# Optimization experiments

Hardware: AMD Instinct MI355X
Metric: run time of the kernel (lower is better)

The kernel has to match this reference:

```python
import jax, jax.numpy as jnp
import numpy as np

N_NODES = 200000
N_EVENTS = 200000
MEM_DIM = 128
MSG_DIM = 128
TIME_DIM = 16
MSG_IN = 2 * MEM_DIM + MSG_DIM + TIME_DIM  # 400


def setup_inputs() -> dict:
    key = jax.random.key(0)
    ks = jax.random.split(key, 12)
    return {
        "src_ids": jax.random.randint(ks[0], (N_EVENTS,), 0, N_NODES, dtype=jnp.int32),
        "dst_ids": jax.random.randint(ks[1], (N_EVENTS,), 0, N_NODES, dtype=jnp.int32),
        "edge_feat": jax.random.normal(ks[2], (N_EVENTS, MSG_DIM), dtype=jnp.float32),
        "timestamps": jax.random.uniform(ks[3], (N_EVENTS,), dtype=jnp.float32),
        "memory": jax.random.normal(ks[4], (N_NODES, MEM_DIM), dtype=jnp.float32) * 0.1,
        "last_update_time": jnp.zeros((N_NODES,), dtype=jnp.float32),
        "time_w": jax.random.normal(ks[5], (TIME_DIM,), dtype=jnp.float32),
        "time_phi": jnp.zeros((TIME_DIM,), dtype=jnp.float32),
        "W1": jax.random.normal(ks[6], (MSG_IN, MSG_DIM), dtype=jnp.float32) / np.sqrt(MSG_IN),
        "b1": jnp.zeros((MSG_DIM,), dtype=jnp.float32),
        "W2": jax.random.normal(ks[7], (MSG_DIM, MSG_DIM), dtype=jnp.float32) / np.sqrt(MSG_DIM),
        "b2": jnp.zeros((MSG_DIM,), dtype=jnp.float32),
        "W_ih": jax.random.normal(ks[8], (3 * MEM_DIM, MSG_DIM), dtype=jnp.float32) / np.sqrt(MSG_DIM),
        "W_hh": jax.random.normal(ks[9], (3 * MEM_DIM, MEM_DIM), dtype=jnp.float32) / np.sqrt(MEM_DIM),
        "b_ih": jnp.zeros((3 * MEM_DIM,), dtype=jnp.float32),
        "b_hh": jnp.zeros((3 * MEM_DIM,), dtype=jnp.float32),
    }


def _time_encode(dt, w, phi):
    # Time2Vec: linear first channel, sin on the rest
    wt = dt[:, None] * w[None, :] + phi[None, :]  # [E, TIME_DIM]
    return jnp.concatenate([wt[:, :1], jnp.sin(wt[:, 1:])], axis=-1)


def _message_mlp(x, W1, b1, W2, b2):
    h = jax.nn.relu(x @ W1 + b1)
    return h @ W2 + b2


def _gru_cell(x, h, W_ih, W_hh, b_ih, b_hh):
    gi = x @ W_ih.T + b_ih  # [U, 3H]
    gh = h @ W_hh.T + b_hh
    i_r, i_z, i_n = jnp.split(gi, 3, axis=-1)
    h_r, h_z, h_n = jnp.split(gh, 3, axis=-1)
    r = jax.nn.sigmoid(i_r + h_r)
    z = jax.nn.sigmoid(i_z + h_z)
    n = jnp.tanh(i_n + r * h_n)
    return (1.0 - z) * n + z * h


def reference(src_ids, dst_ids, edge_feat, timestamps, memory, last_update_time,
              time_w, time_phi, W1, b1, W2, b2, W_ih, W_hh, b_ih, b_hh):
    # 1) gather + time encode
    dt_src = timestamps - last_update_time[src_ids]
    dt_dst = timestamps - last_update_time[dst_ids]
    te_src = _time_encode(dt_src, time_w, time_phi)
    te_dst = _time_encode(dt_dst, time_w, time_phi)
    src_mem = memory[src_ids]
    dst_mem = memory[dst_ids]

    # 2) messages
    msg_src = _message_mlp(jnp.concatenate([src_mem, dst_mem, edge_feat, te_src], -1), W1, b1, W2, b2)
    msg_dst = _message_mlp(jnp.concatenate([dst_mem, src_mem, edge_feat, te_dst], -1), W1, b1, W2, b2)

    all_nodes = jnp.concatenate([src_ids, dst_ids])  # [2E]
    all_msgs = jnp.concatenate([msg_src, msg_dst], axis=0)  # [2E, MSG_DIM]

    # 3) 'last' aggregation: segment-max of positions, then gather
    pos = jnp.arange(all_nodes.shape[0], dtype=jnp.int32)
    last_pos = jax.ops.segment_max(pos, all_nodes, num_segments=N_NODES)  # int32 min where absent
    present = last_pos >= 0  # [N]
    agg = all_msgs[jnp.clip(last_pos, 0, None)]  # [N, MSG_DIM]
    agg = jnp.where(present[:, None], agg, 0.0)

    # 4) GRU memory update on involved nodes only
    new_mem = _gru_cell(agg, memory, W_ih, W_hh, b_ih, b_hh)
    memory_out = jnp.where(present[:, None], new_mem, memory)
    return memory_out
```

## Files before the change

### kernel.cpp

```cpp
#include <hip/hip_runtime.h>
#include <hip/hip_bf16.h>
#include <math.h>

#define NN 200000
#define NE 200000

typedef __attribute__((ext_vector_type(8))) short bf16x8;
typedef __attribute__((ext_vector_type(4))) float f32x4;

#define XASTR 136
#define XBSTR 296
#define OSTR  132
#define NT    (NN / 32)
#define PBT   (32 * XBSTR)

__device__ __forceinline__ float sigm(float x) { return 1.0f / (1.0f + __expf(-x)); }
__device__ __forceinline__ float tanh_f(float x) {
    float e = __expf(2.0f * x);
    return 1.0f - 2.0f / (e + 1.0f);
}
__device__ __forceinline__ ushort f2b(float x) {
    union { __hip_bfloat16 b; ushort u; } v;
    v.b = __float2bfloat16(x);
    return v.u;
}
__device__ __forceinline__ float b2f(ushort u) {
    return __uint_as_float(((unsigned)u) << 16);
}
__device__ __forceinline__ ushort4 cvt4(float4 v) {
    ushort4 u; u.x = f2b(v.x); u.y = f2b(v.y); u.z = f2b(v.z); u.w = f2b(v.w);
    return u;
}
__device__ __forceinline__ void gload_lds16(const ushort* g, ushort* l) {
    __builtin_amdgcn_global_load_lds(
        (const __attribute__((address_space(1))) unsigned int*)g,
        (__attribute__((address_space(3))) unsigned int*)l, 16, 0, 0);
}

#define MFMA16(a, b, c) __builtin_amdgcn_mfma_f32_16x16x32_bf16((a), (b), (c), 0, 0, 0)

__global__ void k_prep(const float* __restrict__ W1, const float* __restrict__ W2,
                       const float* __restrict__ Wih, const float* __restrict__ Whh,
                       const float* __restrict__ b2, const float* __restrict__ bih,
                       ushort* __restrict__ W1F, ushort* __restrict__ W2IF,
                       ushort* __restrict__ WHF, float* __restrict__ cb) {
    int t = blockIdx.x * 256 + threadIdx.x;
    if (t < 104 * 512) {
        int f = t >> 9, idx = t & 511;
        int lane = idx >> 3, j = idx & 7, c16 = lane & 15, k8 = lane >> 4;
        int wvv = f / 26, r = f % 26, kt = r >> 1, ns = r & 1;
        int col = wvv * 32 + ns * 16 + c16;
        int kk = kt * 32 + k8 * 8 + j;
        W1F[t] = (kk < 400) ? f2b(W1[kk * 128 + col]) : (ushort)0;
        return;
    }
    t -= 104 * 512;
    if (t < 96 * 512) {
        int f = t >> 9, idx = t & 511;
        int lane = idx >> 3, j = idx & 7, c16 = lane & 15, k8 = lane >> 4;
        int wvv = f / 24, r = f % 24, kt = r / 6, rem = r % 6, g = rem >> 1, ns = rem & 1;
        int col = g * 128 + wvv * 32 + ns * 16 + c16;
        int kk = kt * 32 + k8 * 8 + j;
        float s = 0.0f;
        for (int c = 0; c < 128; ++c) s = fmaf(W2[kk * 128 + c], Wih[col * 128 + c], s);
        W2IF[f * 512 + idx] = f2b(s);
        return;
    }
    t -= 96 * 512;
    if (t < 96 * 512) {
        int f = t >> 9, idx = t & 511;
        int lane = idx >> 3, j = idx & 7, c16 = lane & 15, k8 = lane >> 4;
        int wvv = f / 24, r = f % 24, kt = r / 6, rem = r % 6, g = rem >> 1, ns = rem & 1;
        int col = g * 128 + wvv * 32 + ns * 16 + c16;
        int kk = kt * 32 + k8 * 8 + j;
        WHF[f * 512 + idx] = f2b(Whh[col * 128 + kk]);
        return;
    }
    t -= 96 * 512;
    if (t < 384) {
        float s = bih[t];
        for (int k = 0; k < 128; ++k) s = fmaf(b2[k], Wih[t * 128 + k], s);
        cb[t] = s;
    }
}

__global__ void k_scatter(const int* __restrict__ src, const int* __restrict__ dst,
                          int* __restrict__ last_pos) {
    int i = blockIdx.x * blockDim.x + threadIdx.x;
    if (i < NE) {
        atomicMax(&last_pos[src[i]], i);
    } else if (i < 2 * NE) {
        atomicMax(&last_pos[dst[i - NE]], i);
    }
}

__global__ __launch_bounds__(256)
void k_gath(const int* __restrict__ last_pos,
            const int* __restrict__ src, const int* __restrict__ dst,
            const float* __restrict__ ts, const float* __restrict__ lut,
            const float* __restrict__ mem, const float* __restrict__ ef,
            const float* __restrict__ tw, const float* __restrict__ tphi,
            ushort* __restrict__ PB)
{
    const int wv = threadIdx.x >> 6, lane = threadIdx.x & 63;
    const int n0 = (blockIdx.x * 4 + wv) * 2;
    const int l = lane - 32;
    #pragma unroll
    for (int s = 0; s < 2; ++s) {
        int n = n0 + s;
        int p = last_pos[n];
        if (p < 0) continue;
        int e     = (p < NE) ? p : p - NE;
        int other = (p < NE) ? dst[e] : src[e];
        ushort* xb = PB + (size_t)n * XBSTR;
        if (lane < 32) {
            float4 v = *(const float4*)&mem[(size_t)other * 128 + lane * 4];
            *(ushort4*)&xb[lane * 4] = cvt4(v);
            float val = 0.0f;
            if (lane < 16) {
                float dt = ts[e] - lut[n];
                float wt = fmaf(dt, tw[lane], tphi[lane]);
                val = (lane == 0) ? wt : __sinf(wt);
            }
            xb[256 + lane] = f2b(val);
        } else {
            float4 w = *(const float4*)&ef[(size_t)e * 128 + l * 4];
            *(ushort4*)&xb[128 + l * 4] = cvt4(w);
        }
    }
}

__global__ __launch_bounds__(256, 4)
void k_main5(const ushort* __restrict__ PB, const int* __restrict__ last_pos,
             const float* __restrict__ mem,
             const ushort* __restrict__ W1F, const float* __restrict__ b1,
             const ushort* __restrict__ W2IF, const ushort* __restrict__ WHF,
             const float* __restrict__ cb, const float* __restrict__ bhh,
             float* __restrict__ out)
{
    __shared__ __align__(16) ushort XA[32 * XASTR];
    __shared__ __align__(16) ushort XB[32 * XBSTR + 256];
    __shared__ unsigned char pres[32];

    const int base = blockIdx.x * 32;
    const int tid  = threadIdx.x;
    const int lane = tid & 63;
    const int wv   = tid >> 6;
    const int r16  = lane & 15;
    const int kb   = lane >> 4;

    {
        const ushort* srcPB = PB + (size_t)blockIdx.x * PBT;
        #pragma unroll
        for (int j = 0; j < 5; ++j) {
            int cc = wv + j * 4;
            if (cc < 18) gload_lds16(srcPB + cc * 512 + lane * 8, XB + cc * 512);
            else if (cc == 18 && lane < 32) gload_lds16(srcPB + cc * 512 + lane * 8, XB + cc * 512);
        }
    }
    {
        const float* msrc = mem + (size_t)base * 128;
        #pragma unroll
        for (int k = 0; k < 4; ++k) {
            int i0 = k * 1024 + tid * 4;
            float4 v = *(const float4*)&msrc[i0];
            int row = i0 >> 7, col = i0 & 127;
            *(ushort4*)&XA[row * XASTR + col] = cvt4(v);
        }
        if (tid < 32) pres[tid] = (unsigned char)(last_pos[base + tid] >= 0);
    }
    float b1v[2], brz0[2], brz1[2], binv[2], bhnv[2];
    #pragma unroll
    for (int ns = 0; ns < 2; ++ns) {
        int col = wv * 32 + ns * 16 + r16;
        b1v[ns]  = b1[col];
        brz0[ns] = cb[col] + bhh[col];
        brz1[ns] = cb[128 + col] + bhh[128 + col];
        binv[ns] = cb[256 + col];
        bhnv[ns] = bhh[256 + col];
    }
    const ushort* w1 = W1F  + wv * (26 * 512) + lane * 8;
    const ushort* wI = W2IF + wv * (24 * 512) + lane * 8;
    const ushort* wH = WHF  + wv * (24 * 512) + lane * 8;
    __syncthreads();

    f32x4 c1[2][2] = {};
    {
        const ushort* aA = &XA[r16 * XASTR + kb * 8];
        const ushort* aB = &XB[r16 * XBSTR + kb * 8];
        #pragma unroll
        for (int kt = 0; kt < 13; ++kt) {
            const ushort* ap  = (kt < 4) ? (aA + kt * 32) : (aB + (kt - 4) * 32);
            const int     ast = (kt < 4) ? XASTR : XBSTR;
            bf16x8 A0 = *(const bf16x8*)ap;
            bf16x8 A1 = *(const bf16x8*)(ap + 16 * ast);
            bf16x8 B0 = *(const bf16x8*)(w1 + (kt * 2 + 0) * 512);
            bf16x8 B1 = *(const bf16x8*)(w1 + (kt * 2 + 1) * 512);
            c1[0][0] = MFMA16(A0, B0, c1[0][0]);
            c1[0][1] = MFMA16(A0, B1, c1[0][1]);
            c1[1][0] = MFMA16(A1, B0, c1[1][0]);
            c1[1][1] = MFMA16(A1, B1, c1[1][1]);
        }
    }
    __syncthreads();

    #pragma unroll
    for (int ns = 0; ns < 2; ++ns) {
        int col = wv * 32 + ns * 16 + r16;
        #pragma unroll
        for (int m = 0; m < 2; ++m)
            #pragma unroll
            for (int r = 0; r < 4; ++r)
                XB[(m * 16 + kb * 4 + r) * XBSTR + col] =
                    f2b(fmaxf(c1[m][ns][r] + b1v[ns], 0.0f));
    }
    __syncthreads();

    f32x4 arz[2][4] = {};
    f32x4 an_i[2][2] = {};
    f32x4 an_h[2][2] = {};
    {
        const ushort* am = &XB[r16 * XBSTR + kb * 8];
        const ushort* ah = &XA[r16 * XASTR + kb * 8];
        #pragma unroll
        for (int kt = 0; kt < 4; ++kt) {
            bf16x8 M0 = *(const bf16x8*)(am + kt * 32);
            bf16x8 M1 = *(const bf16x8*)(am + 16 * XBSTR + kt * 32);
            bf16x8 H0 = *(const bf16x8*)(ah + kt * 32);
            bf16x8 H1 = *(const bf16x8*)(ah + 16 * XASTR + kt * 32);
            #pragma unroll
            for (int g = 0; g < 2; ++g)
                #pragma unroll
                for (int ns = 0; ns < 2; ++ns) {
                    int fo = (kt * 6 + g * 2 + ns) * 512;
                    bf16x8 Bi = *(const bf16x8*)(wI + fo);
                    bf16x8 Bh = *(const bf16x8*)(wH + fo);
                    arz[0][g * 2 + ns] = MFMA16(M0, Bi, arz[0][g * 2 + ns]);
                    arz[0][g * 2 + ns] = MFMA16(H0, Bh, arz[0][g * 2 + ns]);
                    arz[1][g * 2 + ns] = MFMA16(M1, Bi, arz[1][g * 2 + ns]);
                    arz[1][g * 2 + ns] = MFMA16(H1, Bh, arz[1][g * 2 + ns]);
                }
            #pragma unroll
            for (int ns = 0; ns < 2; ++ns) {
                int fo = (kt * 6 + 4 + ns) * 512;
                bf16x8 Bi = *(const bf16x8*)(wI + fo);
                bf16x8 Bh = *(const bf16x8*)(wH + fo);
                an_i[0][ns] = MFMA16(M0, Bi, an_i[0][ns]);
                an_i[1][ns] = MFMA16(M1, Bi, an_i[1][ns]);
                an_h[0][ns] = MFMA16(H0, Bh, an_h[0][ns]);
                an_h[1][ns] = MFMA16(H1, Bh, an_h[1][ns]);
            }
        }
    }
    __syncthreads();

    float* XBf = (float*)XB;
    #pragma unroll
    for (int ns = 0; ns < 2; ++ns) {
        int col = wv * 32 + ns * 16 + r16;
        #pragma unroll
        for (int m = 0; m < 2; ++m) {
            #pragma unroll
            for (int r = 0; r < 4; ++r) {
                int row = m * 16 + kb * 4 + r;
                float rr = sigm(arz[m][0 + ns][r] + brz0[ns]);
                float zz = sigm(arz[m][2 + ns][r] + brz1[ns]);
                float nn = tanh_f(an_i[m][ns][r] + binv[ns] +
                                  rr * (an_h[m][ns][r] + bhnv[ns]));
                float hh = b2f(XA[row * XASTR + col]);
                XBf[row * OSTR + col] = (1.0f - zz) * nn + zz * hh;
            }
        }
    }
    __syncthreads();

    for (int j = wv; j < 32; j += 4) {
        float2 v;
        if (pres[j]) v = *(const float2*)&XBf[j * OSTR + lane * 2];
        else         v = *(const float2*)&mem[(size_t)(base + j) * 128 + lane * 2];
        *(float2*)&out[(size_t)(base + j) * 128 + lane * 2] = v;
    }
}

extern "C" void kernel_launch(void* const* d_in, const int* in_sizes, int n_in,
                              void* d_out, int out_size, void* d_ws, size_t ws_size,
                              hipStream_t stream) {
    const int*   src  = (const int*)d_in[0];
    const int*   dst  = (const int*)d_in[1];
    const float* ef   = (const float*)d_in[2];
    const float* ts   = (const float*)d_in[3];
    const float* mem  = (const float*)d_in[4];
    const float* lut  = (const float*)d_in[5];
    const float* tw   = (const float*)d_in[6];
    const float* tphi = (const float*)d_in[7];
    const float* W1   = (const float*)d_in[8];
    const float* b1   = (const float*)d_in[9];
    const float* W2   = (const float*)d_in[10];
    const float* b2   = (const float*)d_in[11];
    const float* Wih  = (const float*)d_in[12];
    const float* Whh  = (const float*)d_in[13];
    const float* bih  = (const float*)d_in[14];
    const float* bhh  = (const float*)d_in[15];
    float* out = (float*)d_out;

    char* ws = (char*)d_ws;
    size_t off = 0;
    int*    last_pos = (int*)(ws + off);    off += (size_t)NN * 4;
    ushort* W1F      = (ushort*)(ws + off); off += (size_t)104 * 512 * 2;
    ushort* W2IF     = (ushort*)(ws + off); off += (size_t)96 * 512 * 2;
    ushort* WHF      = (ushort*)(ws + off); off += (size_t)96 * 512 * 2;
    float*  cb       = (float*)(ws + off);  off += (size_t)384 * 4 + 64;
    ushort* PB       = (ushort*)(ws + off);

    hipMemsetAsync(last_pos, 0xFF, (size_t)NN * sizeof(int), stream);

    k_prep<<<(104 * 512 + 2 * 96 * 512 + 384 + 255) / 256, 256, 0, stream>>>(
        W1, W2, Wih, Whh, b2, bih, W1F, W2IF, WHF, cb);
    k_scatter<<<(2 * NE + 255) / 256, 256, 0, stream>>>(src, dst, last_pos);
    k_gath<<<NN / 8, 256, 0, stream>>>(last_pos, src, dst, ts, lut, mem, ef, tw, tphi, PB);
    k_main5<<<NT, 256, 0, stream>>>(PB, last_pos, mem, W1F, b1, W2IF, WHF, cb, bhh, out);
}
```

Measured before the change: 270.5 us.

## Merge prep and scatter kernels, double GRU tile rows, write output directly

Folds the weight-prep and scatter kernels into one launch, saving a kernel launch and letting the two overlap. The main GRU kernel now handles 64 rows per block with 512 threads: two row halves share the same column-slice weights, which halves how often global weight fragments are loaded per row. The GRU epilogue writes results straight to global memory, masked by presence, rather than staging them in LDS and copying afterward, which removes a barrier and an LDS round trip. The cost is more LDS per block and therefore possibly lower occupancy, plus uncoalesced scalar output stores.

Result: slower. 279.5 us (+3.3%).

```diff
diff --git a/kernel.cpp b/kernel.cpp
--- a/kernel.cpp
+++ b/kernel.cpp
@@ -10,9 +10,9 @@
 
 #define XASTR 136
 #define XBSTR 296
-#define OSTR  132
-#define NT    (NN / 32)
-#define PBT   (32 * XBSTR)
+#define MROWS 64
+#define NT    (NN / MROWS)
+#define PBT   (MROWS * XBSTR)
 
 __device__ __forceinline__ float sigm(float x) { return 1.0f / (1.0f + __expf(-x)); }
 __device__ __forceinline__ float tanh_f(float x) {
@@ -39,12 +39,26 @@
 
 #define MFMA16(a, b, c) __builtin_amdgcn_mfma_f32_16x16x32_bf16((a), (b), (c), 0, 0, 0)
 
-__global__ void k_prep(const float* __restrict__ W1, const float* __restrict__ W2,
-                       const float* __restrict__ Wih, const float* __restrict__ Whh,
-                       const float* __restrict__ b2, const float* __restrict__ bih,
-                       ushort* __restrict__ W1F, ushort* __restrict__ W2IF,
-                       ushort* __restrict__ WHF, float* __restrict__ cb) {
-    int t = blockIdx.x * 256 + threadIdx.x;
+#define NB_PREP 594
+#define NB_SCAT (((2 * NE) + 255) / 256)
+__global__ void k_pre(const float* __restrict__ W1, const float* __restrict__ W2,
+                      const float* __restrict__ Wih, const float* __restrict__ Whh,
+                      const float* __restrict__ b2, const float* __restrict__ bih,
+                      ushort* __restrict__ W1F, ushort* __restrict__ W2IF,
+                      ushort* __restrict__ WHF, float* __restrict__ cb,
+                      const int* __restrict__ src, const int* __restrict__ dst,
+                      int* __restrict__ last_pos) {
+    int b = blockIdx.x;
+    if (b >= NB_PREP) {
+        int i = (b - NB_PREP) * 256 + threadIdx.x;
+        if (i < NE) {
+            atomicMax(&last_pos[src[i]], i);
+        } else if (i < 2 * NE) {
+            atomicMax(&last_pos[dst[i - NE]], i);
+        }
+        return;
+    }
+    int t = b * 256 + threadIdx.x;
     if (t < 104 * 512) {
         int f = t >> 9, idx = t & 511;
         int lane = idx >> 3, j = idx & 7, c16 = lane & 15, k8 = lane >> 4;
@@ -81,16 +95,6 @@
         float s = bih[t];
         for (int k = 0; k < 128; ++k) s = fmaf(b2[k], Wih[t * 128 + k], s);
         cb[t] = s;
-    }
-}
-
-__global__ void k_scatter(const int* __restrict__ src, const int* __restrict__ dst,
-                          int* __restrict__ last_pos) {
-    int i = blockIdx.x * blockDim.x + threadIdx.x;
-    if (i < NE) {
-        atomicMax(&last_pos[src[i]], i);
-    } else if (i < 2 * NE) {
-        atomicMax(&last_pos[dst[i - NE]], i);
     }
 }
 
@@ -130,22 +134,24 @@
     }
 }
 
-__global__ __launch_bounds__(256, 4)
-void k_main5(const ushort* __restrict__ PB, const int* __restrict__ last_pos,
+__global__ __launch_bounds__(512, 4)
+void k_main6(const ushort* __restrict__ PB, const int* __restrict__ last_pos,
              const float* __restrict__ mem,
              const ushort* __restrict__ W1F, const float* __restrict__ b1,
              const ushort* __restrict__ W2IF, const ushort* __restrict__ WHF,
              const float* __restrict__ cb, const float* __restrict__ bhh,
              float* __restrict__ out)
 {
-    __shared__ __align__(16) ushort XA[32 * XASTR];
-    __shared__ __align__(16) ushort XB[32 * XBSTR + 256];
-    __shared__ unsigned char pres[32];
-
-    const int base = blockIdx.x * 32;
+    __shared__ __align__(16) ushort XA[MROWS * XASTR];
+    __shared__ __align__(16) ushort XB[MROWS * XBSTR];
+    __shared__ unsigned char pres[MROWS];
+
+    const int base = blockIdx.x * MROWS;
     const int tid  = threadIdx.x;
     const int lane = tid & 63;
     const int wv   = tid >> 6;
+    const int cs   = wv & 3;
+    const int row0 = (wv >> 2) * 32;
     const int r16  = lane & 15;
     const int kb   = lane >> 4;
 
@@ -153,41 +159,30 @@
         const ushort* srcPB = PB + (size_t)blockIdx.x * PBT;
         #pragma unroll
         for (int j = 0; j < 5; ++j) {
-            int cc = wv + j * 4;
-            if (cc < 18) gload_lds16(srcPB + cc * 512 + lane * 8, XB + cc * 512);
-            else if (cc == 18 && lane < 32) gload_lds16(srcPB + cc * 512 + lane * 8, XB + cc * 512);
+            int cc = wv + j * 8;
+            if (cc < 37) gload_lds16(srcPB + cc * 512 + lane * 8, XB + cc * 512);
         }
     }
     {
         const float* msrc = mem + (size_t)base * 128;
         #pragma unroll
         for (int k = 0; k < 4; ++k) {
-            int i0 = k * 1024 + tid * 4;
+            int i0 = k * 2048 + tid * 4;
             float4 v = *(const float4*)&msrc[i0];
             int row = i0 >> 7, col = i0 & 127;
             *(ushort4*)&XA[row * XASTR + col] = cvt4(v);
         }
-        if (tid < 32) pres[tid] = (unsigned char)(last_pos[base + tid] >= 0);
-    }
-    float b1v[2], brz0[2], brz1[2], binv[2], bhnv[2];
-    #pragma unroll
-    for (int ns = 0; ns < 2; ++ns) {
-        int col = wv * 32 + ns * 16 + r16;
-        b1v[ns]  = b1[col];
-        brz0[ns] = cb[col] + bhh[col];
-        brz1[ns] = cb[128 + col] + bhh[128 + col];
-        binv[ns] = cb[256 + col];
-        bhnv[ns] = bhh[256 + col];
-    }
-    const ushort* w1 = W1F  + wv * (26 * 512) + lane * 8;
-    const ushort* wI = W2IF + wv * (24 * 512) + lane * 8;
-    const ushort* wH = WHF  + wv * (24 * 512) + lane * 8;
+        if (tid < MROWS) pres[tid] = (unsigned char)(last_pos[base + tid] >= 0);
+    }
+    const ushort* w1 = W1F  + cs * (26 * 512) + lane * 8;
+    const ushort* wI = W2IF + cs * (24 * 512) + lane * 8;
+    const ushort* wH = WHF  + cs * (24 * 512) + lane * 8;
     __syncthreads();
 
     f32x4 c1[2][2] = {};
     {
-        const ushort* aA = &XA[r16 * XASTR + kb * 8];
-        const ushort* aB = &XB[r16 * XBSTR + kb * 8];
+        const ushort* aA = &XA[(row0 + r16) * XASTR + kb * 8];
+        const ushort* aB = &XB[(row0 + r16) * XBSTR + kb * 8];
         #pragma unroll
         for (int kt = 0; kt < 13; ++kt) {
             const ushort* ap  = (kt < 4) ? (aA + kt * 32) : (aB + (kt - 4) * 32);
@@ -206,13 +201,14 @@
 
     #pragma unroll
     for (int ns = 0; ns < 2; ++ns) {
-        int col = wv * 32 + ns * 16 + r16;
+        int col = cs * 32 + ns * 16 + r16;
+        float bb = b1[col];
         #pragma unroll
         for (int m = 0; m < 2; ++m)
             #pragma unroll
             for (int r = 0; r < 4; ++r)
-                XB[(m * 16 + kb * 4 + r) * XBSTR + col] =
-                    f2b(fmaxf(c1[m][ns][r] + b1v[ns], 0.0f));
+                XB[(row0 + m * 16 + kb * 4 + r) * XBSTR + col] =
+                    f2b(fmaxf(c1[m][ns][r] + bb, 0.0f));
     }
     __syncthreads();
 
@@ -220,8 +216,8 @@
     f32x4 an_i[2][2] = {};
     f32x4 an_h[2][2] = {};
     {
-        const ushort* am = &XB[r16 * XBSTR + kb * 8];
-        const ushort* ah = &XA[r16 * XASTR + kb * 8];
+        const ushort* am = &XB[(row0 + r16) * XBSTR + kb * 8];
+        const ushort* ah = &XA[(row0 + r16) * XASTR + kb * 8];
         #pragma unroll
         for (int kt = 0; kt < 4; ++kt) {
             bf16x8 M0 = *(const bf16x8*)(am + kt * 32);
@@ -252,33 +248,35 @@
             }
         }
     }
-    __syncthreads();
-
-    float* XBf = (float*)XB;
+
     #pragma unroll
     for (int ns = 0; ns < 2; ++ns) {
-        int col = wv * 32 + ns * 16 + r16;
+        int col = cs * 32 + ns * 16 + r16;
+        float brz0 = cb[col] + bhh[col];
+        float brz1 = cb[128 + col] + bhh[128 + col];
+        float bin  = cb[256 + col];
+        float bhn  = bhh[256 + col];
         #pragma unroll
         for (int m = 0; m < 2; ++m) {
             #pragma unroll
             for (int r = 0; r < 4; ++r) {
-                int row = m * 16 + kb * 4 + r;
-                float rr = sigm(arz[m][0 + ns][r] + brz0[ns]);
-                float zz = sigm(arz[m][2 + ns][r] + brz1[ns]);
-                float nn = tanh_f(an_i[m][ns][r] + binv[ns] +
-                                  rr * (an_h[m][ns][r] + bhnv[ns]));
-                float hh = b2f(XA[row * XASTR + col]);
-                XBf[row * OSTR + col] = (1.0f - zz) * nn + zz * hh;
+                int row = row0 + m * 16 + kb * 4 + r;
+                if (pres[row]) {
+                    float rr = sigm(arz[m][0 + ns][r] + brz0);
+                    float zz = sigm(arz[m][2 + ns][r] + brz1);
+                    float nn = tanh_f(an_i[m][ns][r] + bin +
+                                      rr * (an_h[m][ns][r] + bhn));
+                    float hh = b2f(XA[row * XASTR + col]);
+                    out[(size_t)(base + row) * 128 + col] = (1.0f - zz) * nn + zz * hh;
+                }
             }
         }
     }
-    __syncthreads();
-
-    for (int j = wv; j < 32; j += 4) {
-        float2 v;
-        if (pres[j]) v = *(const float2*)&XBf[j * OSTR + lane * 2];
-        else         v = *(const float2*)&mem[(size_t)(base + j) * 128 + lane * 2];
-        *(float2*)&out[(size_t)(base + j) * 128 + lane * 2] = v;
+    for (int j = wv; j < MROWS; j += 8) {
+        if (!pres[j]) {
+            float2 v = *(const float2*)&mem[(size_t)(base + j) * 128 + lane * 2];
+            *(float2*)&out[(size_t)(base + j) * 128 + lane * 2] = v;
+        }
     }
 }
 
@@ -314,9 +312,8 @@
 
     hipMemsetAsync(last_pos, 0xFF, (size_t)NN * sizeof(int), stream);
 
-    k_prep<<<(104 * 512 + 2 * 96 * 512 + 384 + 255) / 256, 256, 0, stream>>>(
-        W1, W2, Wih, Whh, b2, bih, W1F, W2IF, WHF, cb);
-    k_scatter<<<(2 * NE + 255) / 256, 256, 0, stream>>>(src, dst, last_pos);
+    k_pre<<<NB_PREP + NB_SCAT, 256, 0, stream>>>(
+        W1, W2, Wih, Whh, b2, bih, W1F, W2IF, WHF, cb, src, dst, last_pos);
     k_gath<<<NN / 8, 256, 0, stream>>>(last_pos, src, dst, ts, lut, mem, ef, tw, tphi, PB);
-    k_main5<<<NT, 256, 0, stream>>>(PB, last_pos, mem, W1F, b1, W2IF, WHF, cb, bhh, out);
-}
+    k_main6<<<NT, 512, 0, stream>>>(PB, last_pos, mem, W1F, b1, W2IF, WHF, cb, bhh, out);
+}
```

## Fuse weight prep with scatter, batch gather loads, add separate hidden LDS buffer

Applied to the files above, without the earlier changes.

Merges the weight-prep kernel and the atomicMax scatter into one launch using block-index ranges, removing one kernel launch and its serialization gap. The gather kernel now issues both nodes' loads before doing any stores, raising memory-level parallelism. The main kernel writes the MLP hidden activations to a dedicated LDS buffer, which lets it drop two __syncthreads barriers, and it moves the bias loads closer to where they are used. The cost is extra LDS per block, which may lower occupancy.

Result: faster. 248.4 us (-8.2%).

```diff
diff --git a/kernel.cpp b/kernel.cpp
--- a/kernel.cpp
+++ b/kernel.cpp
@@ -39,12 +39,26 @@
 
 #define MFMA16(a, b, c) __builtin_amdgcn_mfma_f32_16x16x32_bf16((a), (b), (c), 0, 0, 0)
 
-__global__ void k_prep(const float* __restrict__ W1, const float* __restrict__ W2,
-                       const float* __restrict__ Wih, const float* __restrict__ Whh,
-                       const float* __restrict__ b2, const float* __restrict__ bih,
-                       ushort* __restrict__ W1F, ushort* __restrict__ W2IF,
-                       ushort* __restrict__ WHF, float* __restrict__ cb) {
-    int t = blockIdx.x * 256 + threadIdx.x;
+#define NB_PREP 594
+#define NB_SCAT (((2 * NE) + 255) / 256)
+__global__ void k_pre(const float* __restrict__ W1, const float* __restrict__ W2,
+                      const float* __restrict__ Wih, const float* __restrict__ Whh,
+                      const float* __restrict__ b2, const float* __restrict__ bih,
+                      ushort* __restrict__ W1F, ushort* __restrict__ W2IF,
+                      ushort* __restrict__ WHF, float* __restrict__ cb,
+                      const int* __restrict__ src, const int* __restrict__ dst,
+                      int* __restrict__ last_pos) {
+    int b = blockIdx.x;
+    if (b >= NB_PREP) {
+        int i = (b - NB_PREP) * 256 + threadIdx.x;
+        if (i < NE) {
+            atomicMax(&last_pos[src[i]], i);
+        } else if (i < 2 * NE) {
+            atomicMax(&last_pos[dst[i - NE]], i);
+        }
+        return;
+    }
+    int t = b * 256 + threadIdx.x;
     if (t < 104 * 512) {
         int f = t >> 9, idx = t & 511;
         int lane = idx >> 3, j = idx & 7, c16 = lane & 15, k8 = lane >> 4;
@@ -84,16 +98,6 @@
     }
 }
 
-__global__ void k_scatter(const int* __restrict__ src, const int* __restrict__ dst,
-                          int* __restrict__ last_pos) {
-    int i = blockIdx.x * blockDim.x + threadIdx.x;
-    if (i < NE) {
-        atomicMax(&last_pos[src[i]], i);
-    } else if (i < 2 * NE) {
-        atomicMax(&last_pos[dst[i - NE]], i);
-    }
-}
-
 __global__ __launch_bounds__(256)
 void k_gath(const int* __restrict__ last_pos,
             const int* __restrict__ src, const int* __restrict__ dst,
@@ -104,34 +108,66 @@
 {
     const int wv = threadIdx.x >> 6, lane = threadIdx.x & 63;
     const int n0 = (blockIdx.x * 4 + wv) * 2;
-    const int l = lane - 32;
-    #pragma unroll
-    for (int s = 0; s < 2; ++s) {
-        int n = n0 + s;
-        int p = last_pos[n];
-        if (p < 0) continue;
-        int e     = (p < NE) ? p : p - NE;
-        int other = (p < NE) ? dst[e] : src[e];
-        ushort* xb = PB + (size_t)n * XBSTR;
-        if (lane < 32) {
-            float4 v = *(const float4*)&mem[(size_t)other * 128 + lane * 4];
-            *(ushort4*)&xb[lane * 4] = cvt4(v);
-            float val = 0.0f;
-            if (lane < 16) {
-                float dt = ts[e] - lut[n];
-                float wt = fmaf(dt, tw[lane], tphi[lane]);
-                val = (lane == 0) ? wt : __sinf(wt);
+    const int n1 = n0 + 1;
+    const int l = lane & 31;
+    const bool lo = lane < 32;
+
+    const int p0 = last_pos[n0];
+    const int p1 = last_pos[n1];
+
+    float4 m0, f0, m1, f1;
+    float te0 = 0.0f, te1 = 0.0f;
+    if (p0 >= 0) {
+        int e = (p0 < NE) ? p0 : p0 - NE;
+        int o = (p0 < NE) ? dst[e] : src[e];
+        if (lo) {
+            m0 = *(const float4*)&mem[(size_t)o * 128 + l * 4];
+            if (l < 16) {
+                float dt = ts[e] - lut[n0];
+                float w = fmaf(dt, tw[l], tphi[l]);
+                te0 = (l == 0) ? w : __sinf(w);
             }
-            xb[256 + lane] = f2b(val);
         } else {
-            float4 w = *(const float4*)&ef[(size_t)e * 128 + l * 4];
-            *(ushort4*)&xb[128 + l * 4] = cvt4(w);
+            f0 = *(const float4*)&ef[(size_t)e * 128 + l * 4];
+        }
+    }
+    if (p1 >= 0) {
+        int e = (p1 < NE) ? p1 : p1 - NE;
+        int o = (p1 < NE) ? dst[e] : src[e];
+        if (lo) {
+            m1 = *(const float4*)&mem[(size_t)o * 128 + l * 4];
+            if (l < 16) {
+                float dt = ts[e] - lut[n1];
+                float w = fmaf(dt, tw[l], tphi[l]);
+                te1 = (l == 0) ? w : __sinf(w);
+            }
+        } else {
+            f1 = *(const float4*)&ef[(size_t)e * 128 + l * 4];
+        }
+    }
+
+    if (p0 >= 0) {
+        ushort* xb = PB + (size_t)n0 * XBSTR;
+        if (lo) {
+            *(ushort4*)&xb[l * 4] = cvt4(m0);
+            xb[256 + l] = (l < 16) ? f2b(te0) : (ushort)0;
+        } else {
+            *(ushort4*)&xb[128 + l * 4] = cvt4(f0);
+        }
+    }
+    if (p1 >= 0) {
+        ushort* xb = PB + (size_t)n1 * XBSTR;
+        if (lo) {
+            *(ushort4*)&xb[l * 4] = cvt4(m1);
+            xb[256 + l] = (l < 16) ? f2b(te1) : (ushort)0;
+        } else {
+            *(ushort4*)&xb[128 + l * 4] = cvt4(f1);
         }
     }
 }
 
 __global__ __launch_bounds__(256, 4)
-void k_main5(const ushort* __restrict__ PB, const int* __restrict__ last_pos,
+void k_main7(const ushort* __restrict__ PB, const int* __restrict__ last_pos,
              const float* __restrict__ mem,
              const ushort* __restrict__ W1F, const float* __restrict__ b1,
              const ushort* __restrict__ W2IF, const ushort* __restrict__ WHF,
@@ -139,7 +175,8 @@
              float* __restrict__ out)
 {
     __shared__ __align__(16) ushort XA[32 * XASTR];
-    __shared__ __align__(16) ushort XB[32 * XBSTR + 256];
+    __shared__ __align__(16) ushort HB[32 * XASTR];
+    __shared__ __align__(16) ushort XB[32 * XBSTR];
     __shared__ unsigned char pres[32];
 
     const int base = blockIdx.x * 32;
@@ -164,20 +201,9 @@
         for (int k = 0; k < 4; ++k) {
             int i0 = k * 1024 + tid * 4;
             float4 v = *(const float4*)&msrc[i0];
-            int row = i0 >> 7, col = i0 & 127;
-            *(ushort4*)&XA[row * XASTR + col] = cvt4(v);
+            *(ushort4*)&XA[(i0 >> 7) * XASTR + (i0 & 127)] = cvt4(v);
         }
         if (tid < 32) pres[tid] = (unsigned char)(last_pos[base + tid] >= 0);
-    }
-    float b1v[2], brz0[2], brz1[2], binv[2], bhnv[2];
-    #pragma unroll
-    for (int ns = 0; ns < 2; ++ns) {
-        int col = wv * 32 + ns * 16 + r16;
-        b1v[ns]  = b1[col];
-        brz0[ns] = cb[col] + bhh[col];
-        brz1[ns] = cb[128 + col] + bhh[128 + col];
-        binv[ns] = cb[256 + col];
-        bhnv[ns] = bhh[256 + col];
     }
     const ushort* w1 = W1F  + wv * (26 * 512) + lane * 8;
     const ushort* wI = W2IF + wv * (24 * 512) + lane * 8;
@@ -202,17 +228,16 @@
             c1[1][1] = MFMA16(A1, B1, c1[1][1]);
         }
     }
-    __syncthreads();
-
     #pragma unroll
     for (int ns = 0; ns < 2; ++ns) {
         int col = wv * 32 + ns * 16 + r16;
+        float bb = b1[col];
         #pragma unroll
         for (int m = 0; m < 2; ++m)
             #pragma unroll
             for (int r = 0; r < 4; ++r)
-                XB[(m * 16 + kb * 4 + r) * XBSTR + col] =
-                    f2b(fmaxf(c1[m][ns][r] + b1v[ns], 0.0f));
+                HB[(m * 16 + kb * 4 + r) * XASTR + col] =
+                    f2b(fmaxf(c1[m][ns][r] + bb, 0.0f));
     }
     __syncthreads();
 
@@ -220,12 +245,12 @@
     f32x4 an_i[2][2] = {};
     f32x4 an_h[2][2] = {};
     {
-        const ushort* am = &XB[r16 * XBSTR + kb * 8];
+        const ushort* am = &HB[r16 * XASTR + kb * 8];
         const ushort* ah = &XA[r16 * XASTR + kb * 8];
         #pragma unroll
         for (int kt = 0; kt < 4; ++kt) {
             bf16x8 M0 = *(const bf16x8*)(am + kt * 32);
-            bf16x8 M1 = *(const bf16x8*)(am + 16 * XBSTR + kt * 32);
+            bf16x8 M1 = *(const bf16x8*)(am + 16 * XASTR + kt * 32);
             bf16x8 H0 = *(const bf16x8*)(ah + kt * 32);
             bf16x8 H1 = *(const bf16x8*)(ah + 16 * XASTR + kt * 32);
             #pragma unroll
@@ -252,21 +277,24 @@
             }
         }
     }
-    __syncthreads();
 
     float* XBf = (float*)XB;
     #pragma unroll
     for (int ns = 0; ns < 2; ++ns) {
         int col = wv * 32 + ns * 16 + r16;
+        float brz0 = cb[col] + bhh[col];
+        float brz1 = cb[128 + col] + bhh[128 + col];
+        float bin  = cb[256 + col];
+        float bhn  = bhh[256 + col];
         #pragma unroll
         for (int m = 0; m < 2; ++m) {
             #pragma unroll
             for (int r = 0; r < 4; ++r) {
                 int row = m * 16 + kb * 4 + r;
-                float rr = sigm(arz[m][0 + ns][r] + brz0[ns]);
-                float zz = sigm(arz[m][2 + ns][r] + brz1[ns]);
-                float nn = tanh_f(an_i[m][ns][r] + binv[ns] +
-                                  rr * (an_h[m][ns][r] + bhnv[ns]));
+                float rr = sigm(arz[m][0 + ns][r] + brz0);
+                float zz = sigm(arz[m][2 + ns][r] + brz1);
+                float nn = tanh_f(an_i[m][ns][r] + bin +
+                                  rr * (an_h[m][ns][r] + bhn));
                 float hh = b2f(XA[row * XASTR + col]);
                 XBf[row * OSTR + col] = (1.0f - zz) * nn + zz * hh;
             }
@@ -314,9 +342,8 @@
 
     hipMemsetAsync(last_pos, 0xFF, (size_t)NN * sizeof(int), stream);
 
-    k_prep<<<(104 * 512 + 2 * 96 * 512 + 384 + 255) / 256, 256, 0, stream>>>(
-        W1, W2, Wih, Whh, b2, bih, W1F, W2IF, WHF, cb);
-    k_scatter<<<(2 * NE + 255) / 256, 256, 0, stream>>>(src, dst, last_pos);
+    k_pre<<<NB_PREP + NB_SCAT, 256, 0, stream>>>(
+        W1, W2, Wih, Whh, b2, bih, W1F, W2IF, WHF, cb, src, dst, last_pos);
     k_gath<<<NN / 8, 256, 0, stream>>>(last_pos, src, dst, ts, lut, mem, ef, tw, tphi, PB);
-    k_main5<<<NT, 256, 0, stream>>>(PB, last_pos, mem, W1F, b1, W2IF, WHF, cb, bhh, out);
-}
+    k_main7<<<NT, 256, 0, stream>>>(PB, last_pos, mem, W1F, b1, W2IF, WHF, cb, bhh, out);
+}
```
